# Kernel tuning notes

Hardware: AMD Instinct MI355X
Metric: run time of the kernel (lower is better)

## Reference

```python
import jax, jax.numpy as jnp
import numpy as np

PARTS = (0.0, 0.25, 0.5, 0.75, 1.0)
N = 16777216


def setup_inputs() -> dict:
    key = jax.random.key(0)
    kx, ky, kd = jax.random.split(key, 3)
    x = jax.random.normal(kx, (N, 2), dtype=jnp.float32)
    y = jax.random.normal(ky, (N, 2), dtype=jnp.float32)
    dist = jax.random.uniform(kd, (N,), dtype=jnp.float32)
    return {"x": x, "y": y, "dist": dist}


def _complex_abs(v):
    # fastmri.complex_abs: sqrt(re^2 + im^2) over last dim of size 2
    return jnp.sqrt(jnp.sum(v * v, axis=-1))


def reference(x, y, dist):
    # Per-element squared errors computed once, then masked-reduced per radial bin.
    diff2_sum = jnp.sum((x - y) ** 2, axis=-1)        # [N] sum over the 2 components
    abs_diff2 = (_complex_abs(x) - _complex_abs(y)) ** 2  # [N]

    loss = jnp.float32(0.0)
    for i in range(len(PARTS) - 1):
        r0, r1 = PARTS[i], PARTS[i + 1]
        mask = (dist >= r0) & (dist <= r1)            # inclusive both ends, as in torch code
        cnt = jnp.sum(mask)                           # number of selected points
        # mse over x[ind] of shape [cnt, 2] -> divide by 2*cnt elements
        mse = jnp.sum(jnp.where(mask, diff2_sum, 0.0)) / jnp.maximum(2 * cnt, 1)
        mse_abs = jnp.sum(jnp.where(mask, abs_diff2, 0.0)) / jnp.maximum(cnt, 1)
        loss = loss + jnp.where(cnt > 0, mse + 0.1 * mse_abs, 0.0)
    return loss
```

## Files before the change

### kernel.cpp

```cpp
#include <hip/hip_runtime.h>

#define NBINS 4
#define BLOCK 256
#define UNROLL 4
#define WAVES_PER_BLOCK (BLOCK / 64)
#define NBLOCKS 2048

struct WS {
    float sum_d2[NBINS];
    float sum_ad2[NBINS];
    unsigned int cnt[NBINS];
};

__device__ __forceinline__ void accum_point(float x0, float x1, float y0, float y1,
                                            float d,
                                            float (&s_d2)[NBINS], float (&s_ad2)[NBINS],
                                            unsigned int (&s_cnt)[NBINS]) {
    float dx0 = x0 - y0, dx1 = x1 - y1;
    float d2 = dx0 * dx0 + dx1 * dx1;
    float ax = sqrtf(x0 * x0 + x1 * x1);
    float ay = sqrtf(y0 * y0 + y1 * y1);
    float da = ax - ay;
    float ad2 = da * da;
    const float bounds[NBINS + 1] = {0.0f, 0.25f, 0.5f, 0.75f, 1.0f};
#pragma unroll
    for (int b = 0; b < NBINS; ++b) {
        if (d >= bounds[b] && d <= bounds[b + 1]) {
            s_d2[b] += d2;
            s_ad2[b] += ad2;
            s_cnt[b] += 1u;
        }
    }
}

__global__ __launch_bounds__(BLOCK) void radial_loss_main(
    const float* __restrict__ x, const float* __restrict__ y,
    const float* __restrict__ dist, WS* __restrict__ ws, int n) {
    float s_d2[NBINS] = {0.f, 0.f, 0.f, 0.f};
    float s_ad2[NBINS] = {0.f, 0.f, 0.f, 0.f};
    unsigned int s_cnt[NBINS] = {0u, 0u, 0u, 0u};

    const int n2 = n >> 1;
    const float4* __restrict__ x4 = (const float4*)x;
    const float4* __restrict__ y4 = (const float4*)y;
    const float2* __restrict__ dd2 = (const float2*)dist;

    const int chunk = (n2 + NBLOCKS - 1) / NBLOCKS;
    const int start = blockIdx.x * chunk;
    const int end = min(start + chunk, n2);

    int i = start + threadIdx.x;
    for (; i + (UNROLL - 1) * BLOCK < end; i += UNROLL * BLOCK) {
        float4 xv[UNROLL], yv[UNROLL];
        float2 dv[UNROLL];
#pragma unroll
        for (int u = 0; u < UNROLL; ++u) xv[u] = x4[i + u * BLOCK];
#pragma unroll
        for (int u = 0; u < UNROLL; ++u) yv[u] = y4[i + u * BLOCK];
#pragma unroll
        for (int u = 0; u < UNROLL; ++u) dv[u] = dd2[i + u * BLOCK];
#pragma unroll
        for (int u = 0; u < UNROLL; ++u) {
            accum_point(xv[u].x, xv[u].y, yv[u].x, yv[u].y, dv[u].x, s_d2, s_ad2, s_cnt);
            accum_point(xv[u].z, xv[u].w, yv[u].z, yv[u].w, dv[u].y, s_d2, s_ad2, s_cnt);
        }
    }
    for (; i < end; i += BLOCK) {
        float4 xv = x4[i];
        float4 yv = y4[i];
        float2 dv = dd2[i];
        accum_point(xv.x, xv.y, yv.x, yv.y, dv.x, s_d2, s_ad2, s_cnt);
        accum_point(xv.z, xv.w, yv.z, yv.w, dv.y, s_d2, s_ad2, s_cnt);
    }
    if (blockIdx.x == 0) {
        for (int p = (n2 << 1) + threadIdx.x; p < n; p += BLOCK) {
            accum_point(x[2 * p], x[2 * p + 1], y[2 * p], y[2 * p + 1], dist[p],
                        s_d2, s_ad2, s_cnt);
        }
    }

#pragma unroll
    for (int off = 32; off > 0; off >>= 1) {
#pragma unroll
        for (int b = 0; b < NBINS; ++b) {
            s_d2[b] += __shfl_down(s_d2[b], off);
            s_ad2[b] += __shfl_down(s_ad2[b], off);
            s_cnt[b] += __shfl_down(s_cnt[b], off);
        }
    }

    __shared__ float sm_d2[WAVES_PER_BLOCK][NBINS];
    __shared__ float sm_ad2[WAVES_PER_BLOCK][NBINS];
    __shared__ unsigned int sm_cnt[WAVES_PER_BLOCK][NBINS];
    const int wave = threadIdx.x >> 6;
    const int lane = threadIdx.x & 63;
    if (lane == 0) {
#pragma unroll
        for (int b = 0; b < NBINS; ++b) {
            sm_d2[wave][b] = s_d2[b];
            sm_ad2[wave][b] = s_ad2[b];
            sm_cnt[wave][b] = s_cnt[b];
        }
    }
    __syncthreads();
    if (threadIdx.x < NBINS) {
        const int b = threadIdx.x;
        float td2 = 0.f, tad2 = 0.f;
        unsigned int tc = 0u;
#pragma unroll
        for (int w = 0; w < WAVES_PER_BLOCK; ++w) {
            td2 += sm_d2[w][b];
            tad2 += sm_ad2[w][b];
            tc += sm_cnt[w][b];
        }
        atomicAdd(&ws->sum_d2[b], td2);
        atomicAdd(&ws->sum_ad2[b], tad2);
        atomicAdd(&ws->cnt[b], tc);
    }
}

__global__ void radial_loss_final(const WS* __restrict__ ws, float* __restrict__ out) {
    if (threadIdx.x == 0 && blockIdx.x == 0) {
        float loss = 0.f;
#pragma unroll
        for (int b = 0; b < NBINS; ++b) {
            unsigned int c = ws->cnt[b];
            if (c > 0u) {
                float fc = (float)c;
                loss += ws->sum_d2[b] / (2.0f * fc) + 0.1f * (ws->sum_ad2[b] / fc);
            }
        }
        out[0] = loss;
    }
}

extern "C" void kernel_launch(void* const* d_in, const int* in_sizes, int n_in,
                              void* d_out, int out_size, void* d_ws, size_t ws_size,
                              hipStream_t stream) {
    const float* x = (const float*)d_in[0];
    const float* y = (const float*)d_in[1];
    const float* dist = (const float*)d_in[2];
    float* out = (float*)d_out;
    WS* ws = (WS*)d_ws;
    const int n = in_sizes[2];

    hipMemsetAsync(ws, 0, sizeof(WS), stream);
    radial_loss_main<<<NBLOCKS, BLOCK, 0, stream>>>(x, y, dist, ws, n);
    radial_loss_final<<<1, 64, 0, stream>>>(ws, out);
}
```

Measured before the change: 330.9 us.

## Fold loss terms per point, use branchless disjoint bin masks, fuse final reduction

Each point now contributes a single combined value (0.5*d2 + 0.1*ad2) to one of four disjoint bins, selected by branchless float masks, and counts are kept as floats. This halves the accumulators and shuffle traffic. The separate finalize kernel is replaced by a last-block-done pattern using an atomic counter, which saves one launch. Risks: boundary points (d exactly 0.25, 0.5 or 0.75) were counted in two bins by the inclusive reference and now go to one, and float counts lose exactness above 2^24.

```diff
diff --git a/kernel.cpp b/kernel.cpp
--- a/kernel.cpp
+++ b/kernel.cpp
@@ -7,38 +7,43 @@
 #define NBLOCKS 2048
 
 struct WS {
-    float sum_d2[NBINS];
-    float sum_ad2[NBINS];
-    unsigned int cnt[NBINS];
+    float sum_v[NBINS];
+    float cnt[NBINS];
+    unsigned int done;
 };
 
 __device__ __forceinline__ void accum_point(float x0, float x1, float y0, float y1,
                                             float d,
-                                            float (&s_d2)[NBINS], float (&s_ad2)[NBINS],
-                                            unsigned int (&s_cnt)[NBINS]) {
+                                            float (&acc)[NBINS], float (&cnt)[NBINS]) {
     float dx0 = x0 - y0, dx1 = x1 - y1;
     float d2 = dx0 * dx0 + dx1 * dx1;
     float ax = sqrtf(x0 * x0 + x1 * x1);
     float ay = sqrtf(y0 * y0 + y1 * y1);
     float da = ax - ay;
-    float ad2 = da * da;
-    const float bounds[NBINS + 1] = {0.0f, 0.25f, 0.5f, 0.75f, 1.0f};
-#pragma unroll
-    for (int b = 0; b < NBINS; ++b) {
-        if (d >= bounds[b] && d <= bounds[b + 1]) {
-            s_d2[b] += d2;
-            s_ad2[b] += ad2;
-            s_cnt[b] += 1u;
-        }
-    }
+    float v = 0.5f * d2 + 0.1f * (da * da);
+    bool c1 = d < 0.25f;
+    bool c2 = d < 0.5f;
+    bool c3 = d < 0.75f;
+    float m0 = c1 ? 1.0f : 0.0f;
+    float m1 = (c2 && !c1) ? 1.0f : 0.0f;
+    float m2 = (c3 && !c2) ? 1.0f : 0.0f;
+    float m3 = c3 ? 0.0f : 1.0f;
+    acc[0] = fmaf(v, m0, acc[0]);
+    acc[1] = fmaf(v, m1, acc[1]);
+    acc[2] = fmaf(v, m2, acc[2]);
+    acc[3] = fmaf(v, m3, acc[3]);
+    cnt[0] += m0;
+    cnt[1] += m1;
+    cnt[2] += m2;
+    cnt[3] += m3;
 }
 
-__global__ __launch_bounds__(BLOCK) void radial_loss_main(
+__global__ __launch_bounds__(BLOCK, 4) void radial_loss_main(
     const float* __restrict__ x, const float* __restrict__ y,
-    const float* __restrict__ dist, WS* __restrict__ ws, int n) {
-    float s_d2[NBINS] = {0.f, 0.f, 0.f, 0.f};
-    float s_ad2[NBINS] = {0.f, 0.f, 0.f, 0.f};
-    unsigned int s_cnt[NBINS] = {0u, 0u, 0u, 0u};
+    const float* __restrict__ dist, WS* __restrict__ ws,
+    float* __restrict__ out, int n) {
+    float acc[NBINS] = {0.f, 0.f, 0.f, 0.f};
+    float cnt[NBINS] = {0.f, 0.f, 0.f, 0.f};
 
     const int n2 = n >> 1;
     const float4* __restrict__ x4 = (const float4*)x;
@@ -61,21 +66,21 @@
         for (int u = 0; u < UNROLL; ++u) dv[u] = dd2[i + u * BLOCK];
 #pragma unroll
         for (int u = 0; u < UNROLL; ++u) {
-            accum_point(xv[u].x, xv[u].y, yv[u].x, yv[u].y, dv[u].x, s_d2, s_ad2, s_cnt);
-            accum_point(xv[u].z, xv[u].w, yv[u].z, yv[u].w, dv[u].y, s_d2, s_ad2, s_cnt);
+            accum_point(xv[u].x, xv[u].y, yv[u].x, yv[u].y, dv[u].x, acc, cnt);
+            accum_point(xv[u].z, xv[u].w, yv[u].z, yv[u].w, dv[u].y, acc, cnt);
         }
     }
     for (; i < end; i += BLOCK) {
         float4 xv = x4[i];
         float4 yv = y4[i];
         float2 dv = dd2[i];
-        accum_point(xv.x, xv.y, yv.x, yv.y, dv.x, s_d2, s_ad2, s_cnt);
-        accum_point(xv.z, xv.w, yv.z, yv.w, dv.y, s_d2, s_ad2, s_cnt);
+        accum_point(xv.x, xv.y, yv.x, yv.y, dv.x, acc, cnt);
+        accum_point(xv.z, xv.w, yv.z, yv.w, dv.y, acc, cnt);
     }
     if (blockIdx.x == 0) {
         for (int p = (n2 << 1) + threadIdx.x; p < n; p += BLOCK) {
             accum_point(x[2 * p], x[2 * p + 1], y[2 * p], y[2 * p + 1], dist[p],
-                        s_d2, s_ad2, s_cnt);
+                        acc, cnt);
         }
     }
 
@@ -83,54 +88,48 @@
     for (int off = 32; off > 0; off >>= 1) {
 #pragma unroll
         for (int b = 0; b < NBINS; ++b) {
-            s_d2[b] += __shfl_down(s_d2[b], off);
-            s_ad2[b] += __shfl_down(s_ad2[b], off);
-            s_cnt[b] += __shfl_down(s_cnt[b], off);
+            acc[b] += __shfl_down(acc[b], off);
+            cnt[b] += __shfl_down(cnt[b], off);
         }
     }
 
-    __shared__ float sm_d2[WAVES_PER_BLOCK][NBINS];
-    __shared__ float sm_ad2[WAVES_PER_BLOCK][NBINS];
-    __shared__ unsigned int sm_cnt[WAVES_PER_BLOCK][NBINS];
+    __shared__ float sm_v[WAVES_PER_BLOCK][NBINS];
+    __shared__ float sm_c[WAVES_PER_BLOCK][NBINS];
     const int wave = threadIdx.x >> 6;
     const int lane = threadIdx.x & 63;
     if (lane == 0) {
 #pragma unroll
         for (int b = 0; b < NBINS; ++b) {
-            sm_d2[wave][b] = s_d2[b];
-            sm_ad2[wave][b] = s_ad2[b];
-            sm_cnt[wave][b] = s_cnt[b];
+            sm_v[wave][b] = acc[b];
+            sm_c[wave][b] = cnt[b];
         }
     }
     __syncthreads();
     if (threadIdx.x < NBINS) {
         const int b = threadIdx.x;
-        float td2 = 0.f, tad2 = 0.f;
-        unsigned int tc = 0u;
+        float tv = 0.f, tc = 0.f;
 #pragma unroll
         for (int w = 0; w < WAVES_PER_BLOCK; ++w) {
-            td2 += sm_d2[w][b];
-            tad2 += sm_ad2[w][b];
-            tc += sm_cnt[w][b];
+            tv += sm_v[w][b];
+            tc += sm_c[w][b];
         }
-        atomicAdd(&ws->sum_d2[b], td2);
-        atomicAdd(&ws->sum_ad2[b], tad2);
+        atomicAdd(&ws->sum_v[b], tv);
         atomicAdd(&ws->cnt[b], tc);
     }
-}
-
-__global__ void radial_loss_final(const WS* __restrict__ ws, float* __restrict__ out) {
-    if (threadIdx.x == 0 && blockIdx.x == 0) {
-        float loss = 0.f;
+    __threadfence();
+    __syncthreads();
+    if (threadIdx.x == 0) {
+        unsigned int t = atomicAdd(&ws->done, 1u);
+        if (t == (unsigned int)(gridDim.x - 1)) {
+            float loss = 0.f;
 #pragma unroll
-        for (int b = 0; b < NBINS; ++b) {
-            unsigned int c = ws->cnt[b];
-            if (c > 0u) {
-                float fc = (float)c;
-                loss += ws->sum_d2[b] / (2.0f * fc) + 0.1f * (ws->sum_ad2[b] / fc);
+            for (int b = 0; b < NBINS; ++b) {
+                float s = atomicAdd(&ws->sum_v[b], 0.0f);
+                float c = atomicAdd(&ws->cnt[b], 0.0f);
+                if (c > 0.f) loss += s / c;
             }
+            out[0] = loss;
         }
-        out[0] = loss;
     }
 }
 
@@ -145,6 +144,5 @@
     const int n = in_sizes[2];
 
     hipMemsetAsync(ws, 0, sizeof(WS), stream);
-    radial_loss_main<<<NBLOCKS, BLOCK, 0, stream>>>(x, y, dist, ws, n);
-    radial_loss_final<<<1, 64, 0, stream>>>(ws, out);
+    radial_loss_main<<<NBLOCKS, BLOCK, 0, stream>>>(x, y, dist, ws, out, n);
 }
```

After: 671.0 us. +102.8%, slower.
